# Kernel tuning notes

Measured on AMD Instinct MI355X. Metric: run time of the kernel, lower is better.

Reference implementation:

```python
import jax, jax.numpy as jnp
import numpy as np

X_DIM = 64
Y_DIM = 64
U_DIM = 64
BATCH = 32
SEQ_LEN = 2048
DT = 1.0 / 1024.0
EPS = 1e-4


def setup_inputs() -> dict:
    key = jax.random.key(0)
    k_y, k_a, k_c = jax.random.split(key, 3)
    y = jax.random.normal(k_y, (BATCH, SEQ_LEN, Y_DIM), dtype=jnp.float32)
    # parameters, matching the module's initialization (small noise added to A/C for generality)
    A = jnp.diag(-0.01 * (jnp.arange(X_DIM, dtype=jnp.float32) + 1.0)) \
        + 0.001 * jax.random.normal(k_a, (X_DIM, X_DIM), dtype=jnp.float32)
    B = jnp.eye(X_DIM, U_DIM, dtype=jnp.float32) * 0.1
    C = 0.1 * jax.random.normal(k_c, (Y_DIM, X_DIM), dtype=jnp.float32)
    L_Q = jnp.eye(X_DIM, dtype=jnp.float32) * 0.316
    L_R = jnp.eye(U_DIM, dtype=jnp.float32) * 0.316
    L_V = jnp.eye(Y_DIM, dtype=jnp.float32)
    L_Q_proc = jnp.eye(X_DIM, dtype=jnp.float32) * 0.1
    x0_mean = jnp.zeros((X_DIM,), dtype=jnp.float32)
    P0 = jnp.eye(X_DIM, dtype=jnp.float32) * 0.1
    return {"y": y, "A": A, "B": B, "C": C, "L_Q": L_Q, "L_R": L_R,
            "L_V": L_V, "L_Q_proc": L_Q_proc, "x0_mean": x0_mean, "P0": P0}


def _riccati_step(S, H, n):
    # Euler step of the augmented Hamiltonian flow; P = V @ U^{-1}
    S_new = S + DT * (H @ S)
    U, V = S_new[:n], S_new[n:]
    X = V @ jnp.linalg.inv(U)
    return X, S_new


def _forward(y, A, B, C, L_Q, L_R, L_V, L_Q_proc, x0_mean, P0):
    n = A.shape[0]
    u_dim = B.shape[1]
    y_dim = C.shape[0]
    batch, seq_len, _ = y.shape

    Q = L_Q @ L_Q.T
    R = L_R @ L_R.T
    V = L_V @ L_V.T
    Q_proc = L_Q_proc @ L_Q_proc.T

    # normalize observations (torch.std is unbiased -> ddof=1)
    y_mean = y.mean(axis=(0, 1), keepdims=True)
    y_std = y.std(axis=(0, 1), keepdims=True, ddof=1)
    yn = (y - y_mean) / (y_std + EPS)

    # --- LQR Riccati recursion: P_seq, K_seq (sequential scan over time) ---
    R_inv_reg = jnp.linalg.inv(R + EPS * jnp.eye(u_dim, dtype=R.dtype))
    H_care = jnp.block([[A, -B @ jnp.linalg.inv(R) @ B.T],
                        [-Q, -A.T]])  # augmented Hamiltonian (2n, 2n)

    def lqr_step(S, _):
        X, S_new = _riccati_step(S, H_care, n)
        P = 0.5 * (X + X.T)
        K = R_inv_reg @ (B.T @ P)  # (u_dim, n)
        return S_new, (P, K)

    S0 = jnp.concatenate([jnp.eye(n, dtype=Q.dtype), Q], axis=0)  # P0 = Q
    _, (P_seq, K_seq) = jax.lax.scan(lqr_step, S0, None, length=seq_len)

    # --- Kalman filter (sequential scan, data-dependent per-step linear algebra) ---
    V_reg = V + EPS * jnp.eye(y_dim, dtype=V.dtype)
    V_chol = jnp.linalg.cholesky(V_reg)
    log_det_V = 2.0 * jnp.sum(jnp.log(jnp.diagonal(V_chol)))
    Z = jnp.zeros((n, n), dtype=A.dtype)
    LOG_2PI = jnp.log(2.0 * jnp.pi).astype(A.dtype)

    def kf_step(carry, inp):
        x_t, S, ll = carry
        K_t, y_t = inp  # (u_dim, n), (batch, y_dim)
        A_eff = A - B @ K_t
        x_pred = x_t + DT * (x_t @ A_eff.T)  # (batch, n)
        H_t = jnp.block([[A_eff, Q_proc], [Z, -A_eff.T]])
        P_new, S = _riccati_step(S, H_t, n)
        P_pred = 0.5 * (P_new + P_new.T)
        residual = y_t - x_pred @ C.T  # (batch, y_dim)
        CtP = C @ P_pred  # (y_dim, n)
        Sm = CtP @ C.T + V
        S_inv = jnp.linalg.inv(Sm + EPS * jnp.eye(y_dim, dtype=Sm.dtype))
        Kg = CtP.T @ S_inv  # (n, y_dim)
        x_new = x_pred + residual @ Kg.T
        quad = jnp.sum(residual * (residual @ S_inv.T))  # sum_b r^T S_inv r
        ll = ll - 0.5 * (quad + log_det_V + y_dim * LOG_2PI)
        return (x_new, S, ll), x_new

    S0_kf = jnp.concatenate([jnp.eye(n, dtype=P0.dtype), P0], axis=0)
    x0 = jnp.broadcast_to(x0_mean, (batch, n))
    y_t_major = jnp.swapaxes(yn, 0, 1)  # (T, B, y_dim)
    (_, _, ll), x_filt_t = jax.lax.scan(kf_step, (x0, S0_kf, jnp.float32(0.0)),
                                        (K_seq, y_t_major))
    x_filt = jnp.swapaxes(x_filt_t, 0, 1)  # (B, T, n)
    log_likelihood = ll / seq_len

    # controls, prediction, quadratic costs (fully vectorized)
    u_seq = -jnp.einsum('tux,btx->btu', K_seq, x_filt)
    y_pred = x_filt @ C.T
    x_cost = jnp.einsum('btx,xz,btz->b', x_filt, Q, x_filt)
    u_cost = jnp.einsum('btu,uv,btv->b', u_seq, R, u_seq)
    control_cost = jnp.mean(x_cost + u_cost)
    return log_likelihood, control_cost, x_filt, u_seq, y_pred, yn


def reference(y, A, B, C, L_Q, L_R, L_V, L_Q_proc, x0_mean, P0):
    return _forward(y, A, B, C, L_Q, L_R, L_V, L_Q_proc, x0_mean, P0)
```

## Files before the change

kernel.cpp:

```cpp
#include <hip/hip_runtime.h>
#include <math.h>

#define XD 64
#define SEQL 2048
#define NB 32
#define DT_C  (1.0f/1024.0f)
#define EPS_C 1e-4f
#define LD 68
#define LOG2PI 1.8378770664093453f
#define CHUNK 8
#define NCH 256

#define OFF_PARTIAL 0u
#define OFF_MEAN    32768u
#define OFF_STD     32832u
#define OFF_Q       32896u
#define OFF_R       36992u
#define OFF_VM      41088u
#define OFF_QP      45184u
#define OFF_RIREG   49280u
#define OFF_LOGDET  53376u
#define OFF_CHAIN   53440u
#define OFF_POW     250048u
#define OFF_BOUNDS  1298624u
#define OFF_K       1568960u
#define OFF_AEFF    9957568u
#define OFF_UV      18346176u
#define OFF_G       35123392u
#define OFF_B       43512000u
#define OFF_OPS2    OFF_UV
#define OFF_OPS3G   47706304u
#define OFF_OPS3B   49803456u
#define OFF_SB2     50852032u
#define OFF_XB      52949184u
#define OFF_QUAD    53473472u
#define OFF_COST    53475520u
#define OFF_BRI     53541056u

#define OOFF_XF 2
#define OOFF_U  4194306
#define OOFF_YP 8388610
#define OOFF_YN 12582914

template<int KD>
__device__ __forceinline__ void mmNN(int t, float* __restrict__ out, int ldo,
    const float* __restrict__ A, int lda, const float* __restrict__ B, int ldb,
    const float* __restrict__ addC = nullptr, int ldc = 0, float alpha = 1.0f)
{
  const int r0 = (t >> 4) << 2, c0 = (t & 15) << 2;
  float acc[4][4] = {};
  for (int k = 0; k < KD; k += 4) {
    float a_[4][4];
    #pragma unroll
    for (int i = 0; i < 4; ++i) {
      const float4 x = *(const float4*)&A[(r0+i)*lda + k];
      a_[i][0]=x.x; a_[i][1]=x.y; a_[i][2]=x.z; a_[i][3]=x.w;
    }
    #pragma unroll
    for (int kk = 0; kk < 4; ++kk) {
      const float4 bv = *(const float4*)&B[(k+kk)*ldb + c0];
      #pragma unroll
      for (int i = 0; i < 4; ++i) {
        const float a = a_[i][kk];
        acc[i][0] += a*bv.x; acc[i][1] += a*bv.y; acc[i][2] += a*bv.z; acc[i][3] += a*bv.w;
      }
    }
  }
  #pragma unroll
  for (int i = 0; i < 4; ++i)
    #pragma unroll
    for (int j = 0; j < 4; ++j) {
      float v = alpha*acc[i][j];
      if (addC) v += addC[(r0+i)*ldc + (c0+j)];
      out[(r0+i)*ldo + (c0+j)] = v;
    }
}

template<int KD>
__device__ __forceinline__ void mmTA(int t, float* __restrict__ out, int ldo,
    const float* __restrict__ A, int lda, const float* __restrict__ B, int ldb,
    const float* __restrict__ addC = nullptr, int ldc = 0, float alpha = 1.0f)
{
  const int r0 = (t >> 4) << 2, c0 = (t & 15) << 2;
  float acc[4][4] = {};
  for (int k = 0; k < KD; k += 4) {
    #pragma unroll
    for (int kk = 0; kk < 4; ++kk) {
      const float4 av4 = *(const float4*)&A[(k+kk)*lda + r0];
      const float4 bv4 = *(const float4*)&B[(k+kk)*ldb + c0];
      const float av[4] = {av4.x, av4.y, av4.z, av4.w};
      const float bv[4] = {bv4.x, bv4.y, bv4.z, bv4.w};
      #pragma unroll
      for (int i = 0; i < 4; ++i)
        #pragma unroll
        for (int j = 0; j < 4; ++j)
          acc[i][j] += av[i]*bv[j];
    }
  }
  #pragma unroll
  for (int i = 0; i < 4; ++i)
    #pragma unroll
    for (int j = 0; j < 4; ++j) {
      float v = alpha*acc[i][j];
      if (addC) v += addC[(r0+i)*ldc + (c0+j)];
      out[(r0+i)*ldo + (c0+j)] = v;
    }
}

template<int KD>
__device__ __forceinline__ void mmTB(int t, float* __restrict__ out, int ldo,
    const float* __restrict__ A, int lda, const float* __restrict__ B, int ldb,
    const float* __restrict__ addC = nullptr, int ldc = 0, float alpha = 1.0f)
{
  const int r0 = (t >> 4) << 2, c0 = (t & 15) << 2;
  float acc[4][4] = {};
  for (int k = 0; k < KD; k += 4) {
    float a_[4][4], b_[4][4];
    #pragma unroll
    for (int i = 0; i < 4; ++i) {
      const float4 x = *(const float4*)&A[(r0+i)*lda + k];
      a_[i][0]=x.x; a_[i][1]=x.y; a_[i][2]=x.z; a_[i][3]=x.w;
    }
    #pragma unroll
    for (int j = 0; j < 4; ++j) {
      const float4 x = *(const float4*)&B[(c0+j)*ldb + k];
      b_[j][0]=x.x; b_[j][1]=x.y; b_[j][2]=x.z; b_[j][3]=x.w;
    }
    #pragma unroll
    for (int i = 0; i < 4; ++i)
      #pragma unroll
      for (int j = 0; j < 4; ++j)
        acc[i][j] += a_[i][0]*b_[j][0] + a_[i][1]*b_[j][1] + a_[i][2]*b_[j][2] + a_[i][3]*b_[j][3];
  }
  #pragma unroll
  for (int i = 0; i < 4; ++i)
    #pragma unroll
    for (int j = 0; j < 4; ++j) {
      float v = alpha*acc[i][j];
      if (addC) v += addC[(r0+i)*ldc + (c0+j)];
      out[(r0+i)*ldo + (c0+j)] = v;
    }
}

__device__ __forceinline__ void symTile(int t, float* __restrict__ outb, const float* __restrict__ X)
{
  const int r0 = (t >> 4) << 2, c0 = (t & 15) << 2;
  float xa[4][4], xb[4][4];
  #pragma unroll
  for (int i = 0; i < 4; ++i) {
    const float4 u = *(const float4*)&X[(r0+i)*LD + c0];
    xa[i][0]=u.x; xa[i][1]=u.y; xa[i][2]=u.z; xa[i][3]=u.w;
    const float4 v = *(const float4*)&X[(c0+i)*LD + r0];
    xb[i][0]=v.x; xb[i][1]=v.y; xb[i][2]=v.z; xb[i][3]=v.w;
  }
  #pragma unroll
  for (int i = 0; i < 4; ++i) {
    float4 o;
    o.x = 0.5f*(xa[i][0] + xb[0][i]);
    o.y = 0.5f*(xa[i][1] + xb[1][i]);
    o.z = 0.5f*(xa[i][2] + xb[2][i]);
    o.w = 0.5f*(xa[i][3] + xb[3][i]);
    *(float4*)&outb[(r0+i)*LD + c0] = o;
  }
}

template<int KD>
__device__ __forceinline__ void mm32NN(int t, float* __restrict__ out, int ldo,
    const float* __restrict__ A, int lda, const float* __restrict__ B, int ldb,
    const float* __restrict__ addC = nullptr, int ldc = 0, float alpha = 1.0f)
{
  const int r0 = (t >> 4) << 1, c0 = (t & 15) << 2;
  float acc[2][4] = {};
  for (int k = 0; k < KD; k += 4) {
    float a_[2][4];
    #pragma unroll
    for (int i = 0; i < 2; ++i) {
      const float4 x = *(const float4*)&A[(r0+i)*lda + k];
      a_[i][0]=x.x; a_[i][1]=x.y; a_[i][2]=x.z; a_[i][3]=x.w;
    }
    #pragma unroll
    for (int kk = 0; kk < 4; ++kk) {
      const float4 bv = *(const float4*)&B[(k+kk)*ldb + c0];
      #pragma unroll
      for (int i = 0; i < 2; ++i) {
        const float a = a_[i][kk];
        acc[i][0] += a*bv.x; acc[i][1] += a*bv.y; acc[i][2] += a*bv.z; acc[i][3] += a*bv.w;
      }
    }
  }
  #pragma unroll
  for (int i = 0; i < 2; ++i)
    #pragma unroll
    for (int j = 0; j < 4; ++j) {
      float v = alpha*acc[i][j];
      if (addC) v += addC[(r0+i)*ldc + (c0+j)];
      out[(r0+i)*ldo + (c0+j)] = v;
    }
}

template<int KD>
__device__ __forceinline__ void mm32TB(int t, float* __restrict__ out, int ldo,
    const float* __restrict__ A, size_t lda, const float* __restrict__ B, int ldb,
    const float* __restrict__ addC = nullptr, size_t ldc = 0, float alpha = 1.0f)
{
  const int r0 = (t >> 4) << 1, c0 = (t & 15) << 2;
  float acc[2][4] = {};
  for (int k = 0; k < KD; k += 4) {
    float a_[2][4], b_[4][4];
    #pragma unroll
    for (int i = 0; i < 2; ++i) {
      const float4 x = *(const float4*)&A[(size_t)(r0+i)*lda + k];
      a_[i][0]=x.x; a_[i][1]=x.y; a_[i][2]=x.z; a_[i][3]=x.w;
    }
    #pragma unroll
    for (int j = 0; j < 4; ++j) {
      const float4 x = *(const float4*)&B[(c0+j)*ldb + k];
      b_[j][0]=x.x; b_[j][1]=x.y; b_[j][2]=x.z; b_[j][3]=x.w;
    }
    #pragma unroll
    for (int i = 0; i < 2; ++i)
      #pragma unroll
      for (int j = 0; j < 4; ++j)
        acc[i][j] += a_[i][0]*b_[j][0] + a_[i][1]*b_[j][1] + a_[i][2]*b_[j][2] + a_[i][3]*b_[j][3];
  }
  #pragma unroll
  for (int i = 0; i < 2; ++i)
    #pragma unroll
    for (int j = 0; j < 4; ++j) {
      float v = alpha*acc[i][j];
      if (addC) v += addC[(size_t)(r0+i)*ldc + (c0+j)];
      out[(r0+i)*ldo + (c0+j)] = v;
    }
}

__device__ __forceinline__ void gj64(int t, float* __restrict__ Am, float* __restrict__ R)
{
  const int r = t >> 2;
  const int c0 = (t & 3) << 4;
  for (int k = 0; k < 64; ++k) {
    __syncthreads();
    const float pv = Am[k*LD + k];
    const float f = Am[r*LD + k] / pv;
    if (r != k) {
      #pragma unroll
      for (int c = 0; c < 16; c += 4) {
        float4 ak = *(const float4*)&Am[k*LD + c0 + c];
        float4 ar = *(float4*)&Am[r*LD + c0 + c];
        ar.x -= f*ak.x; ar.y -= f*ak.y; ar.z -= f*ak.z; ar.w -= f*ak.w;
        *(float4*)&Am[r*LD + c0 + c] = ar;
        float4 rk = *(const float4*)&R[k*LD + c0 + c];
        float4 rr = *(float4*)&R[r*LD + c0 + c];
        rr.x -= f*rk.x; rr.y -= f*rk.y; rr.z -= f*rk.z; rr.w -= f*rk.w;
        *(float4*)&R[r*LD + c0 + c] = rr;
      }
    }
  }
  __syncthreads();
  const float dinv = 1.0f / Am[r*LD + r];
  #pragma unroll
  for (int c = 0; c < 16; c += 4) {
    float4 rr = *(float4*)&R[r*LD + c0 + c];
    rr.x *= dinv; rr.y *= dinv; rr.z *= dinv; rr.w *= dinv;
    *(float4*)&R[r*LD + c0 + c] = rr;
  }
  __syncthreads();
}

__device__ __forceinline__ void gjb8(int t, float* __restrict__ Am, float* __restrict__ R)
{
  const int r  = t >> 2;
  const int c0 = (t & 3) << 4;
  const int j2 = t >> 5;
  const int cc = (t & 31) << 2;
  const int lane = t & 63;
  const int li = lane >> 3, lj = lane & 7;
  for (int kb = 0; kb < 8; ++kb) {
    const int K = kb << 3;
    __syncthreads();
    const bool inK = ((unsigned)(r - K)) < 8u;
    float4 f0 = make_float4(0.f,0.f,0.f,0.f), f1 = f0;
    if (!inK) {
      f0 = *(const float4*)&Am[r*LD + K];
      f1 = *(const float4*)&Am[r*LD + K + 4];
    }
    float a = Am[(K+li)*LD + K + lj];
    float w = (li == lj) ? 1.0f : 0.0f;
    #pragma unroll
    for (int p = 0; p < 8; ++p) {
      const float pv  = __shfl(a, p*8 + p, 64);
      const float pvr = __builtin_amdgcn_rcpf(pv);
      const float aip = __shfl(a, li*8 + p, 64);
      const float apj = __shfl(a, p*8 + lj, 64);
      const float wpj = __shfl(w, p*8 + lj, 64);
      const float fi  = aip * pvr;
      if (li == p) { a *= pvr; w *= pvr; }
      else         { a -= fi * apj; w -= fi * wpj; }
    }
    float wrow[8];
    #pragma unroll
    for (int m = 0; m < 8; ++m) wrow[m] = __shfl(w, j2*8 + m, 64);
    const int c4 = cc & 63;
    float* srcB = (cc < 64) ? Am : R;
    float4 acc = make_float4(0.f, 0.f, 0.f, 0.f);
    #pragma unroll
    for (int m = 0; m < 8; ++m) {
      const float4 rv = *(const float4*)&srcB[(K+m)*LD + c4];
      acc.x += wrow[m]*rv.x; acc.y += wrow[m]*rv.y; acc.z += wrow[m]*rv.z; acc.w += wrow[m]*rv.w;
    }
    __syncthreads();
    *(float4*)&srcB[(K+j2)*LD + c4] = acc;
    __syncthreads();
    if (!inK) {
      const float fj[8] = {f0.x, f0.y, f0.z, f0.w, f1.x, f1.y, f1.z, f1.w};
      #pragma unroll
      for (int c = 0; c < 16; c += 4) {
        const int cab = c0 + c;
        if (cab >= K + 8) {
          float4 v = *(float4*)&Am[r*LD + cab];
          #pragma unroll
          for (int j = 0; j < 8; ++j) {
            const float4 p4 = *(const float4*)&Am[(K+j)*LD + cab];
            v.x -= fj[j]*p4.x; v.y -= fj[j]*p4.y; v.z -= fj[j]*p4.z; v.w -= fj[j]*p4.w;
          }
          *(float4*)&Am[r*LD + cab] = v;
        }
      }
      #pragma unroll
      for (int c = 0; c < 16; c += 4) {
        const int cab = c0 + c;
        float4 v = *(float4*)&R[r*LD + cab];
        #pragma unroll
        for (int j = 0; j < 8; ++j) {
          const float4 p4 = *(const float4*)&R[(K+j)*LD + cab];
          v.x -= fj[j]*p4.x; v.y -= fj[j]*p4.y; v.z -= fj[j]*p4.z; v.w -= fj[j]*p4.w;
        }
        *(float4*)&R[r*LD + cab] = v;
      }
    }
  }
  __syncthreads();
}


__global__ __launch_bounds__(256) void k_stats(const float* __restrict__ y, float* __restrict__ ws)
{
  __shared__ float sbuf[4][128];
  const int t = threadIdx.x, blk = blockIdx.x;
  const int d = t & 63, g = t >> 6;
  float s = 0.f, s2 = 0.f;
  for (int r = g; r < 256; r += 4) {
    const float v = y[(size_t)(blk*256 + r)*64 + d];
    s += v; s2 += v*v;
  }
  sbuf[g][d] = s; sbuf[g][64+d] = s2;
  __syncthreads();
  if (t < 128) ws[OFF_PARTIAL + (size_t)blk*128 + t] = sbuf[0][t]+sbuf[1][t]+sbuf[2][t]+sbuf[3][t];
}

__global__ __launch_bounds__(256) void k_setup(
    const float* __restrict__ A, const float* __restrict__ Bi,
    const float* __restrict__ LQ, const float* __restrict__ LR,
    const float* __restrict__ LV, const float* __restrict__ LQp,
    float* __restrict__ ws)
{
  __shared__ float b1[64*LD], b2[64*LD], b3[64*LD], b4[64*LD], bQ[64*LD];
  __shared__ float sred[128];
  const int t = threadIdx.x;

  if (t < 128) {
    float acc = 0.f;
    for (int p = 0; p < 256; ++p) acc += ws[OFF_PARTIAL + (size_t)p*128 + t];
    sred[t] = acc;
  }
  __syncthreads();
  if (t < 64) {
    const float mean = sred[t] * (1.0f/65536.0f);
    const float var = (sred[64+t] - 65536.0f*mean*mean) * (1.0f/65535.0f);
    ws[OFF_MEAN + t] = mean;
    ws[OFF_STD + t] = sqrtf(var);
  }

  mmTB<64>(t, bQ, LD, LQ, 64, LQ, 64);
  mmTB<64>(t, b3, LD, LR, 64, LR, 64);
  mmTB<64>(t, ws+OFF_VM, 64, LV, 64, LV, 64);
  mmTB<64>(t, ws+OFF_QP, 64, LQp, 64, LQp, 64);
  __syncthreads();
  for (int idx = t; idx < 4096; idx += 256) {
    const int r = idx>>6, c = idx&63;
    ws[OFF_Q + idx] = bQ[r*LD+c];
    ws[OFF_R + idx] = b3[r*LD+c];
    b1[r*LD+c] = b3[r*LD+c] + ((r==c)?EPS_C:0.f);
    b2[r*LD+c] = (r==c)?1.f:0.f;
  }
  gj64(t, b1, b2);
  mmNN<64>(t, b4, LD, Bi, 64, b2, LD);
  __syncthreads();
  for (int idx = t; idx < 4096; idx += 256) {
    ws[OFF_RIREG + idx] = b2[(idx>>6)*LD+(idx&63)];
    ws[OFF_BRI + idx]   = b4[(idx>>6)*LD+(idx&63)];
  }
  __syncthreads();
  for (int idx = t; idx < 4096; idx += 256) {
    const int r = idx>>6, c = idx&63;
    b1[r*LD+c] = b3[r*LD+c];
    b2[r*LD+c] = (r==c)?1.f:0.f;
  }
  gj64(t, b1, b2);
  mmTB<64>(t, b3, LD, b2, LD, Bi, 64);
  __syncthreads();
  mmNN<64>(t, b4, LD, Bi, 64, b3, LD);
  mmTB<64>(t, b1, LD, LV, 64, LV, 64);
  __syncthreads();
  if (t < 64) b1[t*LD+t] += EPS_C;
  {
    const int r = t >> 2, c0 = (t & 3) << 4;
    float lsum = 0.f;
    for (int k = 0; k < 64; ++k) {
      __syncthreads();
      const float pv = b1[k*LD+k];
      lsum += logf(pv);
      const float f = b1[r*LD+k] / pv;
      if (r != k) {
        #pragma unroll
        for (int c = 0; c < 16; c += 4) {
          float4 ak = *(const float4*)&b1[k*LD+c0+c];
          float4 ar = *(float4*)&b1[r*LD+c0+c];
          ar.x -= f*ak.x; ar.y -= f*ak.y; ar.z -= f*ak.z; ar.w -= f*ak.w;
          *(float4*)&b1[r*LD+c0+c] = ar;
        }
      }
    }
    if (t == 0) ws[OFF_LOGDET] = lsum;
  }
  __syncthreads();
  float* M0 = ws + OFF_CHAIN;
  for (int idx = t; idx < 16384; idx += 256) {
    const int i = idx >> 7, j = idx & 127;
    float v;
    if (i < 64) v = (j < 64) ? (((i==j)?1.f:0.f) + DT_C*A[i*64+j]) : (-DT_C*b4[i*LD + (j-64)]);
    else        v = (j < 64) ? (-DT_C*bQ[(i-64)*LD + j]) : (((i==j)?1.f:0.f) - DT_C*A[(j-64)*64 + (i-64)]);
    M0[idx] = v;
  }
  for (int idx = t; idx < 16384; idx += 256) {
    const int i = idx >> 7, j = idx & 127;
    ws[OFF_POW + idx] = (i==j)?1.f:0.f;
  }
  for (int idx = t; idx < 8192; idx += 256) {
    const int i = idx >> 6, j = idx & 63;
    ws[OFF_BOUNDS + idx] = (i < 64) ? ((i==j)?1.f:0.f) : bQ[(i-64)*LD + j];
  }
}

__global__ __launch_bounds__(256) void k_yn(const float* __restrict__ y, const float* __restrict__ ws, float* __restrict__ out)
{
  const size_t i0 = ((size_t)blockIdx.x*256 + threadIdx.x)*4;
  const int d = (int)(i0 & 63);
  const float4 v = *(const float4*)&y[i0];
  const float4 m = *(const float4*)&ws[OFF_MEAN + d];
  const float4 s = *(const float4*)&ws[OFF_STD + d];
  float* o = out + OOFF_YN + i0;
  o[0] = (v.x - m.x)/(s.x + EPS_C);
  o[1] = (v.y - m.y)/(s.y + EPS_C);
  o[2] = (v.z - m.z)/(s.z + EPS_C);
  o[3] = (v.w - m.w)/(s.w + EPS_C);
}

__global__ __launch_bounds__(256) void k_sq(const float* __restrict__ src, float* __restrict__ dst)
{
  const int t = threadIdx.x;
  const int r = blockIdx.x*8 + (t >> 5);
  const int c0 = (t & 31) << 2;
  float acc[4] = {0.f,0.f,0.f,0.f};
  for (int k = 0; k < 128; k += 4) {
    const float4 a4 = *(const float4*)&src[r*128 + k];
    const float av[4] = {a4.x, a4.y, a4.z, a4.w};
    #pragma unroll
    for (int kk = 0; kk < 4; ++kk) {
      const float4 bv = *(const float4*)&src[(k+kk)*128 + c0];
      acc[0] += av[kk]*bv.x; acc[1] += av[kk]*bv.y; acc[2] += av[kk]*bv.z; acc[3] += av[kk]*bv.w;
    }
  }
  float4 o; o.x=acc[0]; o.y=acc[1]; o.z=acc[2]; o.w=acc[3];
  *(float4*)&dst[r*128 + c0] = o;
}

__global__ __launch_bounds__(256) void k_pow(const float* __restrict__ chainj, float* __restrict__ powt, int level)
{
  const int i = blockIdx.x >> 2, sub = blockIdx.x & 3;
  const float* Bm = powt + (size_t)i*16384;
  float* D = powt + (size_t)(i + (1<<level))*16384;
  const int t = threadIdx.x;
  const int r0 = sub*32 + ((t >> 4) << 1);
  const int c0 = (t & 15) << 3;
  float acc[2][8] = {};
  for (int k = 0; k < 128; k += 4) {
    float a_[2][4];
    {
      const float4 x = *(const float4*)&chainj[r0*128 + k];
      a_[0][0]=x.x; a_[0][1]=x.y; a_[0][2]=x.z; a_[0][3]=x.w;
      const float4 y2 = *(const float4*)&chainj[(r0+1)*128 + k];
      a_[1][0]=y2.x; a_[1][1]=y2.y; a_[1][2]=y2.z; a_[1][3]=y2.w;
    }
    #pragma unroll
    for (int kk = 0; kk < 4; ++kk) {
      const float4 b0 = *(const float4*)&Bm[(k+kk)*128 + c0];
      const float4 b1v = *(const float4*)&Bm[(k+kk)*128 + c0 + 4];
      #pragma unroll
      for (int i2 = 0; i2 < 2; ++i2) {
        const float a = a_[i2][kk];
        acc[i2][0] += a*b0.x; acc[i2][1] += a*b0.y; acc[i2][2] += a*b0.z; acc[i2][3] += a*b0.w;
        acc[i2][4] += a*b1v.x; acc[i2][5] += a*b1v.y; acc[i2][6] += a*b1v.z; acc[i2][7] += a*b1v.w;
      }
    }
  }
  #pragma unroll
  for (int i2 = 0; i2 < 2; ++i2)
    #pragma unroll
    for (int j = 0; j < 8; ++j)
      D[(r0+i2)*128 + c0 + j] = acc[i2][j];
}

__global__ __launch_bounds__(256) void k_boundsk(const float* __restrict__ chainp, float* __restrict__ ws, int level)
{
  const int kb = blockIdx.x >> 1, sub = blockIdx.x & 1;
  const int dsti = kb + (1 << level);
  if (dsti > 32) return;
  const float* S = ws + OFF_BOUNDS + (size_t)kb*8192;
  float* D = ws + OFF_BOUNDS + (size_t)dsti*8192;
  const int t = threadIdx.x;
  const int r0 = sub*64 + ((t >> 4) << 2);
  const int c0 = (t & 15) << 2;
  float acc[4][4] = {};
  for (int k = 0; k < 128; k += 4) {
    float a_[4][4];
    #pragma unroll
    for (int i = 0; i < 4; ++i) {
      const float4 x = *(const float4*)&chainp[(r0+i)*128 + k];
      a_[i][0]=x.x; a_[i][1]=x.y; a_[i][2]=x.z; a_[i][3]=x.w;
    }
    #pragma unroll
    for (int kk = 0; kk < 4; ++kk) {
      const float4 bv = *(const float4*)&S[(k+kk)*64 + c0];
      #pragma unroll
      for (int i = 0; i < 4; ++i) {
        const float a = a_[i][kk];
        acc[i][0] += a*bv.x; acc[i][1] += a*bv.y; acc[i][2] += a*bv.z; acc[i][3] += a*bv.w;
      }
    }
  }
  #pragma unroll
  for (int i = 0; i < 4; ++i)
    #pragma unroll
    for (int j = 0; j < 4; ++j)
      D[(r0+i)*64 + c0 + j] = acc[i][j];
}

__global__ __launch_bounds__(256) void k_lqr(const float* __restrict__ Ain, const float* __restrict__ Bin, float* __restrict__ ws)
{
  __shared__ float b1[64*LD], b2[64*LD], b3[64*LD];
  const int t = threadIdx.x, tt = blockIdx.x;
  const int tp1 = tt + 1, kc = tp1 >> 6, rr = tp1 & 63;
  const float* Mr = ws + OFF_POW + (size_t)rr*16384;
  const float* SB = ws + OFF_BOUNDS + (size_t)kc*8192;
  mmNN<128>(t, b1, LD, Mr, 128, SB, 64);
  mmNN<128>(t, b3, LD, Mr + 8192, 128, SB, 64);
  for (int idx = t; idx < 4096; idx += 256) {
    const int r = idx>>6, c = idx&63;
    b2[r*LD+c] = (r==c)?1.f:0.f;
  }
  gjb8(t, b1, b2);
  mmNN<64>(t, b1, LD, b3, LD, b2, LD);
  __syncthreads();
  symTile(t, b3, b1);
  __syncthreads();
  mmTA<64>(t, b1, LD, Bin, 64, b3, LD);
  __syncthreads();
  mmNN<64>(t, b2, LD, ws+OFF_RIREG, 64, b1, LD);
  mmNN<64>(t, b3, LD, ws+OFF_BRI, 64, b1, LD);
  __syncthreads();
  float* Kout = ws + OFF_K + (size_t)tt*4096;
  float* Ae   = ws + OFF_AEFF + (size_t)tt*4096;
  for (int idx = t; idx < 4096; idx += 256) {
    const int p = (idx>>6)*LD + (idx&63);
    Kout[idx] = b2[p];
    Ae[idx]   = Ain[idx] - b3[p];
  }
}

__global__ __launch_bounds__(1024) void k_ops2(const float* __restrict__ ws_aeff, const float* __restrict__ ws_qp, float* __restrict__ dstE)
{
  __shared__ float E[64*LD], W[64*LD], F[64*LD], T1[64*LD], T2[64*LD], T3[64*LD], T4[64*LD];
  const int t = threadIdx.x, c = blockIdx.x, g = t >> 8, tl = t & 255;
  for (int idx = t; idx < 4096; idx += 1024) {
    const int r = idx>>6, cc = idx&63; const float id = (r==cc)?1.f:0.f;
    E[r*LD+cc] = id; W[r*LD+cc] = 0.f; F[r*LD+cc] = id;
  }
  __syncthreads();
  for (int s = 0; s < CHUNK; ++s) {
    const float* Ae = ws_aeff + ((size_t)c*CHUNK + s)*4096;
    if (g == 0)      mmNN<64>(tl, T1, LD, Ae, 64, E, LD);
    else if (g == 1) mmNN<64>(tl, T2, LD, Ae, 64, W, LD);
    else if (g == 2) mmNN<64>(tl, T3, LD, ws_qp, 64, F, LD);
    else             mmTA<64>(tl, T4, LD, Ae, 64, F, LD);
    __syncthreads();
    for (int idx = t; idx < 4096; idx += 1024) {
      const int p = (idx>>6)*LD + (idx&63);
      E[p] += DT_C*T1[p];
      W[p] += DT_C*(T2[p] + T3[p]);
      F[p] -= DT_C*T4[p];
    }
    __syncthreads();
  }
  float* dst = dstE + (size_t)c*12288;
  for (int idx = t; idx < 4096; idx += 1024) {
    const int p = (idx>>6)*LD + (idx&63);
    dst[idx] = E[p]; dst[4096+idx] = W[p]; dst[8192+idx] = F[p];
  }
}

__global__ __launch_bounds__(1024) void k_scan2(const float* __restrict__ src, float* __restrict__ dst, int s)
{
  __shared__ float t1[64*LD], t2[64*LD];
  const int i = blockIdx.x, t = threadIdx.x, g = t>>8, tl = t&255;
  const float* si = src + (size_t)i*12288;
  float* di = dst + (size_t)i*12288;
  if (i < s) {
    for (int idx = t; idx < 12288; idx += 1024) di[idx] = si[idx];
    return;
  }
  const float* sj = src + (size_t)(i-s)*12288;
  if (g == 0)      mmNN<64>(tl, di, 64, si, 64, sj, 64);
  else if (g == 1) mmNN<64>(tl, t1, LD, si, 64, sj+4096, 64);
  else if (g == 2) mmNN<64>(tl, t2, LD, si+4096, 64, sj+8192, 64);
  else             mmNN<64>(tl, di+8192, 64, si+8192, 64, sj+8192, 64);
  __syncthreads();
  for (int idx = t; idx < 4096; idx += 1024) {
    const int p = (idx>>6)*LD + (idx&63);
    di[4096+idx] = t1[p] + t2[p];
  }
}

__global__ __launch_bounds__(256) void k_sb2(const float* __restrict__ phi, const float* __restrict__ P0, float* __restrict__ ws)
{
  const int c = blockIdx.x, t = threadIdx.x;
  float* D = ws + OFF_SB2 + (size_t)c*8192;
  if (c == 0) {
    for (int idx = t; idx < 4096; idx += 256) {
      const int r = idx>>6, cc = idx&63;
      D[idx] = (r==cc)?1.f:0.f;
      D[4096+idx] = P0[idx];
    }
    return;
  }
  const float* ph = phi + (size_t)(c-1)*12288;
  mmNN<64>(t, D, 64, ph+4096, 64, P0, 64, ph, 64);
  mmNN<64>(t, D+4096, 64, ph+8192, 64, P0, 64);
}

__global__ __launch_bounds__(1024) void k_uvwalk(const float* __restrict__ ws_aeff, const float* __restrict__ ws_qp,
    const float* __restrict__ ws_sb2, float* __restrict__ ws_uv)
{
  __shared__ float U[64*LD], V[64*LD], T1[64*LD], T2[64*LD], T3[64*LD];
  const int c = blockIdx.x, t = threadIdx.x, g = t>>8, tl = t&255;
  const float* S = ws_sb2 + (size_t)c*8192;
  for (int idx = t; idx < 4096; idx += 1024) {
    const int p = (idx>>6)*LD + (idx&63);
    U[p] = S[idx]; V[p] = S[4096+idx];
  }
  __syncthreads();
  for (int s = 0; s < CHUNK; ++s) {
    const size_t tt = (size_t)c*CHUNK + s;
    const float* Ae = ws_aeff + tt*4096;
    if (g == 0)      mmNN<64>(tl, T1, LD, Ae, 64, U, LD);
    else if (g == 1) mmNN<64>(tl, T2, LD, ws_qp, 64, V, LD);
    else if (g == 2) mmTA<64>(tl, T3, LD, Ae, 64, V, LD);
    __syncthreads();
    float* O = ws_uv + tt*8192;
    for (int idx = t; idx < 4096; idx += 1024) {
      const int p = (idx>>6)*LD + (idx&63);
      const float un = U[p] + DT_C*(T1[p] + T2[p]);
      const float vn = V[p] - DT_C*T3[p];
      U[p] = un; V[p] = vn;
      O[idx] = un; O[4096+idx] = vn;
    }
    __syncthreads();
  }
}

__global__ __launch_bounds__(256) void k_kfper(const float* __restrict__ Cin, const float* __restrict__ outyn, float* __restrict__ ws)
{
  __shared__ float b1[64*LD], b2[64*LD], b3[64*LD];
  const int t = threadIdx.x, tt = blockIdx.x;
  float* base = ws + OFF_UV + (size_t)tt*8192;
  for (int idx = t; idx < 4096; idx += 256) {
    const int r = idx>>6, c = idx&63;
    b1[r*LD+c] = base[idx];
    b3[r*LD+c] = base[4096+idx];
    b2[r*LD+c] = (r==c)?1.f:0.f;
  }
  gjb8(t, b1, b2);
  mmNN<64>(t, b1, LD, b3, LD, b2, LD);
  __syncthreads();
  symTile(t, b3, b1);
  __syncthreads();
  mmNN<64>(t, b1, LD, Cin, 64, b3, LD);
  __syncthreads();
  mmTB<64>(t, b2, LD, b1, LD, Cin, 64, ws+OFF_VM, 64);
  __syncthreads();
  if (t < 64) b2[t*LD+t] += EPS_C;
  for (int idx = t; idx < 4096; idx += 256) {
    const int r = idx>>6, c = idx&63;
    b3[r*LD+c] = (r==c)?1.f:0.f;
  }
  gjb8(t, b2, b3);
  for (int idx = t; idx < 4096; idx += 256) base[4096+idx] = b3[(idx>>6)*LD+(idx&63)];
  mmTA<64>(t, b2, LD, b1, LD, b3, LD);
  __syncthreads();
  for (int idx = t; idx < 4096; idx += 256) base[idx] = b2[(idx>>6)*LD+(idx&63)];
  mmNN<64>(t, b3, LD, b2, LD, Cin, 64);
  __syncthreads();
  const float* Ae = ws + OFF_AEFF + (size_t)tt*4096;
  float* Gg = ws + OFF_G + (size_t)tt*4096;
  {
    const int r0 = (t>>4)<<2, cg0 = (t&15)<<2;
    float acc[4][4] = {};
    for (int k = 0; k < 64; k += 4) {
      float a_[4][4];
      #pragma unroll
      for (int kk = 0; kk < 4; ++kk) {
        const float4 x = *(const float4*)&Ae[(k+kk)*64 + r0];
        a_[kk][0]=x.x; a_[kk][1]=x.y; a_[kk][2]=x.z; a_[kk][3]=x.w;
      }
      float yv[4][4];
      #pragma unroll
      for (int j = 0; j < 4; ++j) {
        const float4 z4 = *(const float4*)&b3[(cg0+j)*LD + k];
        yv[j][0] = -z4.x; yv[j][1] = -z4.y; yv[j][2] = -z4.z; yv[j][3] = -z4.w;
        const int dk = (cg0+j) - k;
        if (dk >= 0 && dk < 4) yv[j][dk] += 1.0f;
      }
      #pragma unroll
      for (int kk = 0; kk < 4; ++kk)
        #pragma unroll
        for (int i = 0; i < 4; ++i) {
          const float a = a_[kk][i];
          #pragma unroll
          for (int j = 0; j < 4; ++j) acc[i][j] += a * yv[j][kk];
        }
    }
    #pragma unroll
    for (int i = 0; i < 4; ++i)
      #pragma unroll
      for (int j = 0; j < 4; ++j) {
        const int rw = r0+i, cw = cg0+j;
        const float Yij = ((rw==cw)?1.f:0.f) - b3[cw*LD + rw];
        b1[rw*LD+cw] = Yij + DT_C*acc[i][j];
      }
  }
  __syncthreads();
  for (int idx = t; idx < 4096; idx += 256) Gg[idx] = b1[(idx>>6)*LD+(idx&63)];
  mm32TB<64>(t, b3, LD, outyn + (size_t)tt*64, (size_t)131072, b2, LD);
  __syncthreads();
  float* Bout = ws + OFF_B + (size_t)tt*2048;
  for (int idx = t; idx < 2048; idx += 256) Bout[idx] = b3[(idx>>6)*LD+(idx&63)];
}

__global__ __launch_bounds__(1024) void k_ops3(const float* __restrict__ ws_g, const float* __restrict__ ws_b,
    float* __restrict__ dG, float* __restrict__ dB)
{
  __shared__ float Gc[64*LD], TG[64*LD], bc[NB*LD], Tb[NB*LD];
  const int t = threadIdx.x, c = blockIdx.x, g = t >> 8, tl = t & 255;
  for (int idx = t; idx < 4096; idx += 1024) {
    const int r = idx>>6, cc = idx&63;
    Gc[r*LD+cc] = (r==cc)?1.f:0.f;
  }
  for (int idx = t; idx < 2048; idx += 1024) bc[(idx>>6)*LD+(idx&63)] = 0.f;
  __syncthreads();
  for (int s = 0; s < CHUNK; ++s) {
    const size_t tt = (size_t)c*CHUNK + s;
    const float* Gt = ws_g + tt*4096;
    if (g == 0)      mmNN<64>(tl, TG, LD, Gc, LD, Gt, 64);
    else if (g == 1) mm32NN<64>(tl, Tb, LD, bc, LD, Gt, 64);
    __syncthreads();
    for (int idx = t; idx < 4096; idx += 1024) {
      const int p = (idx>>6)*LD + (idx&63);
      Gc[p] = TG[p];
    }
    const float* bt = ws_b + tt*2048;
    for (int idx = t; idx < 2048; idx += 1024) {
      const int p = (idx>>6)*LD + (idx&63);
      bc[p] = Tb[p] + bt[idx];
    }
    __syncthreads();
  }
  for (int idx = t; idx < 4096; idx += 1024) dG[(size_t)c*4096 + idx] = Gc[(idx>>6)*LD+(idx&63)];
  for (int idx = t; idx < 2048; idx += 1024) dB[(size_t)c*2048 + idx] = bc[(idx>>6)*LD+(idx&63)];
}

__global__ __launch_bounds__(512) void k_scan3(const float* __restrict__ sG, const float* __restrict__ sB,
    float* __restrict__ dG, float* __restrict__ dB, int s)
{
  const int i = blockIdx.x, t = threadIdx.x, g = t>>8, tl = t&255;
  if (i < s) {
    for (int idx = t; idx < 4096; idx += 512) dG[(size_t)i*4096+idx] = sG[(size_t)i*4096+idx];
    for (int idx = t; idx < 2048; idx += 512) dB[(size_t)i*2048+idx] = sB[(size_t)i*2048+idx];
    return;
  }
  const float* Ge = sG + (size_t)(i-s)*4096;
  const float* Gl = sG + (size_t)i*4096;
  if (g == 0) mmNN<64>(tl, dG + (size_t)i*4096, 64, Ge, 64, Gl, 64);
  else        mm32NN<64>(tl, dB + (size_t)i*2048, 64, sB + (size_t)(i-s)*2048, 64, Gl, 64,
                         sB + (size_t)i*2048, 64);
}

__global__ __launch_bounds__(256) void k_xb(const float* __restrict__ phiG, const float* __restrict__ phiB,
    const float* __restrict__ x0, float* __restrict__ ws)
{
  __shared__ float v[64];
  const int c = blockIdx.x, t = threadIdx.x;
  float* D = ws + OFF_XB + (size_t)c*2048;
  if (c == 0) {
    for (int idx = t; idx < 2048; idx += 256) D[idx] = x0[idx&63];
    return;
  }
  const float* G = phiG + (size_t)(c-1)*4096;
  const float* b = phiB + (size_t)(c-1)*2048;
  if (t < 64) {
    float acc = 0.f;
    for (int k = 0; k < 64; ++k) acc += x0[k]*G[k*64 + t];
    v[t] = acc;
  }
  __syncthreads();
  for (int idx = t; idx < 2048; idx += 256) D[idx] = v[idx&63] + b[idx];
}

__global__ __launch_bounds__(256) void k_xwalk(const float* __restrict__ ws_g, const float* __restrict__ ws_b,
    const float* __restrict__ ws_xb, float* __restrict__ outx)
{
  __shared__ float x[NB*LD], xn[NB*LD];
  const int c = blockIdx.x, t = threadIdx.x;
  const float* X0 = ws_xb + (size_t)c*2048;
  for (int idx = t; idx < 2048; idx += 256) x[(idx>>6)*LD+(idx&63)] = X0[idx];
  __syncthreads();
  for (int s = 0; s < CHUNK; ++s) {
    const size_t tt = (size_t)c*CHUNK + s;
    mm32NN<64>(t, xn, LD, x, LD, ws_g + tt*4096, 64, ws_b + tt*2048, 64);
    __syncthreads();
    for (int idx = t; idx < 2048; idx += 256) {
      const int i = idx>>6, d = idx&63;
      const float val = xn[i*LD+d];
      x[i*LD+d] = val;
      outx[(size_t)i*131072 + tt*64 + d] = val;
    }
    __syncthreads();
  }
}

__global__ __launch_bounds__(256) void k_final(const float* __restrict__ Cin, const float* __restrict__ x0,
    const float* __restrict__ outx, const float* __restrict__ outyn,
    float* __restrict__ outu, float* __restrict__ outyp, float* __restrict__ ws)
{
  __shared__ float xc[NB*LD], z[NB*LD], t1[NB*LD], t2[NB*LD];
  __shared__ float red4[4];
  const int tt = blockIdx.x, t = threadIdx.x;
  for (int idx = t; idx < 2048; idx += 256) {
    const int i = idx>>6, d = idx&63;
    xc[i*LD+d] = outx[(size_t)i*131072 + (size_t)tt*64 + d];
    z[i*LD+d]  = (tt == 0) ? x0[d] : outx[(size_t)i*131072 + (size_t)(tt-1)*64 + d];
  }
  __syncthreads();
  mm32TB<64>(t, t1, LD, xc, LD, ws + OFF_K + (size_t)tt*4096, 64, nullptr, 0, -1.0f);
  mm32TB<64>(t, t2, LD, xc, LD, Cin, 64);
  __syncthreads();
  for (int idx = t; idx < 2048; idx += 256) {
    const int i = idx>>6, d = idx&63;
    outu[(size_t)i*131072 + (size_t)tt*64 + d]  = t1[i*LD+d];
    outyp[(size_t)i*131072 + (size_t)tt*64 + d] = t2[i*LD+d];
  }
  __syncthreads();
  mm32NN<64>(t, t2, LD, xc, LD, ws + OFF_Q, 64);
  __syncthreads();
  const int i_ = t >> 3, lane8 = t & 7;
  float cpart = 0.f;
  for (int d = lane8; d < 64; d += 8) cpart += t2[i_*LD+d]*xc[i_*LD+d];
  __syncthreads();
  mm32NN<64>(t, t2, LD, t1, LD, ws + OFF_R, 64);
  __syncthreads();
  for (int d = lane8; d < 64; d += 8) cpart += t2[i_*LD+d]*t1[i_*LD+d];
  cpart += __shfl_down(cpart, 4, 8);
  cpart += __shfl_down(cpart, 2, 8);
  cpart += __shfl_down(cpart, 1, 8);
  if (lane8 == 0) ws[OFF_COST + (size_t)tt*32 + i_] = cpart;
  __syncthreads();
  mm32TB<64>(t, t2, LD, z, LD, ws + OFF_AEFF + (size_t)tt*4096, 64, z, LD, DT_C);
  __syncthreads();
  mm32TB<64>(t, t1, LD, t2, LD, Cin, 64, outyn + (size_t)tt*64, (size_t)131072, -1.0f);
  __syncthreads();
  mm32TB<64>(t, z, LD, t1, LD, ws + OFF_UV + (size_t)tt*8192 + 4096, 64);
  __syncthreads();
  float q = 0.f;
  for (int idx = t; idx < 2048; idx += 256) {
    const int p = (idx>>6)*LD + (idx&63);
    q += t1[p]*z[p];
  }
  q += __shfl_down(q, 32); q += __shfl_down(q, 16); q += __shfl_down(q, 8);
  q += __shfl_down(q, 4);  q += __shfl_down(q, 2);  q += __shfl_down(q, 1);
  if ((t & 63) == 0) red4[t>>6] = q;
  __syncthreads();
  if (t == 0) ws[OFF_QUAD + tt] = red4[0]+red4[1]+red4[2]+red4[3];
}

__global__ __launch_bounds__(256) void k_scalars(const float* __restrict__ ws, float* __restrict__ out)
{
  __shared__ float red[256];
  const int t = threadIdx.x;
  float q = 0.f;
  for (int i = t; i < 2048; i += 256) q += ws[OFF_QUAD + i];
  red[t] = q;
  __syncthreads();
  for (int s = 128; s > 0; s >>= 1) { if (t < s) red[t] += red[t+s]; __syncthreads(); }
  const float quadsum = red[0];
  __syncthreads();
  {
    const int b = t & 31, chunk = t >> 5;
    float a = 0.f;
    for (int j = 0; j < 256; ++j) a += ws[OFF_COST + (size_t)(chunk*256 + j)*32 + b];
    red[t] = a;
  }
  __syncthreads();
  if (t < 32) {
    float a = 0.f;
    for (int ch = 0; ch < 8; ++ch) a += red[ch*32 + t];
    red[t] = a;
  }
  __syncthreads();
  if (t == 0) {
    float cc = 0.f;
    for (int b = 0; b < 32; ++b) cc += red[b];
    out[1] = cc / 32.0f;
    const float ld = ws[OFF_LOGDET];
    out[0] = -0.5f*(quadsum + 2048.0f*(ld + 64.0f*LOG2PI)) / 2048.0f;
  }
}

extern "C" void kernel_launch(void* const* d_in, const int* in_sizes, int n_in,
                              void* d_out, int out_size, void* d_ws, size_t ws_size,
                              hipStream_t stream)
{
  (void)in_sizes; (void)n_in; (void)out_size; (void)ws_size;
  const float* y   = (const float*)d_in[0];
  const float* A   = (const float*)d_in[1];
  const float* Bi  = (const float*)d_in[2];
  const float* C   = (const float*)d_in[3];
  const float* LQ  = (const float*)d_in[4];
  const float* LR  = (const float*)d_in[5];
  const float* LV  = (const float*)d_in[6];
  const float* LQp = (const float*)d_in[7];
  const float* x0  = (const float*)d_in[8];
  const float* P0  = (const float*)d_in[9];
  float* out = (float*)d_out;
  float* ws  = (float*)d_ws;

  k_stats<<<256, 256, 0, stream>>>(y, ws);
  k_setup<<<1, 256, 0, stream>>>(A, Bi, LQ, LR, LV, LQp, ws);
  k_yn<<<4096, 256, 0, stream>>>(y, ws, out);

  for (int j = 1; j <= 11; ++j)
    k_sq<<<16, 256, 0, stream>>>(ws + OFF_CHAIN + (size_t)(j-1)*16384, ws + OFF_CHAIN + (size_t)j*16384);
  for (int j = 0; j <= 5; ++j)
    k_pow<<<4 << j, 256, 0, stream>>>(ws + OFF_CHAIN + (size_t)j*16384, ws + OFF_POW, j);
  for (int j = 0; j <= 5; ++j)
    k_boundsk<<<2 << j, 256, 0, stream>>>(ws + OFF_CHAIN + (size_t)(6+j)*16384, ws, j);

  k_lqr<<<2048, 256, 0, stream>>>(A, Bi, ws);

  k_ops2<<<NCH, 1024, 0, stream>>>(ws + OFF_AEFF, ws + OFF_QP, ws + OFF_OPS2);
  {
    float* pa = ws + OFF_OPS2;
    float* pb = pa + (size_t)NCH*12288;
    float* src = pa; float* dst = pb;
    for (int s = 1; s < NCH; s <<= 1) {
      k_scan2<<<NCH, 1024, 0, stream>>>(src, dst, s);
      float* tmp = src; src = dst; dst = tmp;
    }
    k_sb2<<<NCH, 256, 0, stream>>>(src, P0, ws);
  }
  k_uvwalk<<<NCH, 1024, 0, stream>>>(ws + OFF_AEFF, ws + OFF_QP, ws + OFF_SB2, ws + OFF_UV);
  k_kfper<<<2048, 256, 0, stream>>>(C, out + OOFF_YN, ws);

  k_ops3<<<NCH, 1024, 0, stream>>>(ws + OFF_G, ws + OFF_B, ws + OFF_OPS3G, ws + OFF_OPS3B);
  {
    float* ga = ws + OFF_OPS3G; float* gb = ga + (size_t)NCH*4096;
    float* ba = ws + OFF_OPS3B; float* bb = ba + (size_t)NCH*2048;
    float *gs = ga, *gd = gb, *bs = ba, *bd = bb;
    for (int s = 1; s < NCH; s <<= 1) {
      k_scan3<<<NCH, 512, 0, stream>>>(gs, bs, gd, bd, s);
      float* t1p = gs; gs = gd; gd = t1p;
      float* t2p = bs; bs = bd; bd = t2p;
    }
    k_xb<<<NCH, 256, 0, stream>>>(gs, bs, x0, ws);
  }
  k_xwalk<<<NCH, 256, 0, stream>>>(ws + OFF_G, ws + OFF_B, ws + OFF_XB, out + OOFF_XF);

  k_final<<<2048, 256, 0, stream>>>(C, x0, out + OOFF_XF, out + OOFF_YN, out + OOFF_U, out + OOFF_YP, ws);
  k_scalars<<<1, 256, 0, stream>>>(ws, out);
}
```

Before: 2.356 ms.

## Fuse repeated-squaring chain into one LDS kernel and merge pow/bounds launches

Replaces 11 separate k_sq launches with a single 1024-thread block that keeps the 128x128 matrix in shared memory (128 KB across two buffers) and squares it repeatedly, writing each power to global. It also merges the k_pow and k_boundsk launches for each level into one k_powbounds launch, since the two are independent. This cuts roughly 17 kernel launches and their serialisation gaps. In exchange the squaring runs on a single CU, and it needs 128 KB of LDS, which must fit the device limit.

Result: slower. 2.459 ms (+4.4%).

```diff
diff --git a/kernel.cpp b/kernel.cpp
--- a/kernel.cpp
+++ b/kernel.cpp
@@ -465,94 +465,110 @@
   o[3] = (v.w - m.w)/(s.w + EPS_C);
 }
 
-__global__ __launch_bounds__(256) void k_sq(const float* __restrict__ src, float* __restrict__ dst)
-{
+__global__ __launch_bounds__(1024) void k_sqchain(float* __restrict__ chain)
+{
+  __shared__ float bufA[128*128], bufB[128*128];
   const int t = threadIdx.x;
-  const int r = blockIdx.x*8 + (t >> 5);
-  const int c0 = (t & 31) << 2;
-  float acc[4] = {0.f,0.f,0.f,0.f};
-  for (int k = 0; k < 128; k += 4) {
-    const float4 a4 = *(const float4*)&src[r*128 + k];
-    const float av[4] = {a4.x, a4.y, a4.z, a4.w};
-    #pragma unroll
-    for (int kk = 0; kk < 4; ++kk) {
-      const float4 bv = *(const float4*)&src[(k+kk)*128 + c0];
-      acc[0] += av[kk]*bv.x; acc[1] += av[kk]*bv.y; acc[2] += av[kk]*bv.z; acc[3] += av[kk]*bv.w;
-    }
-  }
-  float4 o; o.x=acc[0]; o.y=acc[1]; o.z=acc[2]; o.w=acc[3];
-  *(float4*)&dst[r*128 + c0] = o;
-}
-
-__global__ __launch_bounds__(256) void k_pow(const float* __restrict__ chainj, float* __restrict__ powt, int level)
-{
-  const int i = blockIdx.x >> 2, sub = blockIdx.x & 3;
-  const float* Bm = powt + (size_t)i*16384;
-  float* D = powt + (size_t)(i + (1<<level))*16384;
+  for (int idx = t; idx < 16384; idx += 1024) bufA[idx] = chain[idx];
+  __syncthreads();
+  float* Abuf = bufA; float* Bbuf = bufB;
+  for (int j = 1; j <= 11; ++j) {
+    float* dst = chain + (size_t)j*16384;
+    const int c0 = (t & 31) << 2;
+    #pragma unroll
+    for (int g = 0; g < 4; ++g) {
+      const int r = (t >> 5) + (g << 5);
+      float a0=0.f, a1=0.f, a2=0.f, a3=0.f;
+      for (int k = 0; k < 128; k += 4) {
+        const float4 a4 = *(const float4*)&Abuf[r*128 + k];
+        const float av[4] = {a4.x, a4.y, a4.z, a4.w};
+        #pragma unroll
+        for (int kk = 0; kk < 4; ++kk) {
+          const float4 b4 = *(const float4*)&Abuf[(k+kk)*128 + c0];
+          a0 += av[kk]*b4.x; a1 += av[kk]*b4.y; a2 += av[kk]*b4.z; a3 += av[kk]*b4.w;
+        }
+      }
+      float4 o; o.x=a0; o.y=a1; o.z=a2; o.w=a3;
+      *(float4*)&Bbuf[r*128 + c0] = o;
+      *(float4*)&dst[r*128 + c0] = o;
+    }
+    __syncthreads();
+    float* tmp = Abuf; Abuf = Bbuf; Bbuf = tmp;
+  }
+}
+
+__global__ __launch_bounds__(256) void k_powbounds(const float* __restrict__ chain, float* __restrict__ ws, int level)
+{
+  const int nbp = 4 << level;
   const int t = threadIdx.x;
-  const int r0 = sub*32 + ((t >> 4) << 1);
-  const int c0 = (t & 15) << 3;
-  float acc[2][8] = {};
-  for (int k = 0; k < 128; k += 4) {
-    float a_[2][4];
-    {
-      const float4 x = *(const float4*)&chainj[r0*128 + k];
-      a_[0][0]=x.x; a_[0][1]=x.y; a_[0][2]=x.z; a_[0][3]=x.w;
-      const float4 y2 = *(const float4*)&chainj[(r0+1)*128 + k];
-      a_[1][0]=y2.x; a_[1][1]=y2.y; a_[1][2]=y2.z; a_[1][3]=y2.w;
-    }
-    #pragma unroll
-    for (int kk = 0; kk < 4; ++kk) {
-      const float4 b0 = *(const float4*)&Bm[(k+kk)*128 + c0];
-      const float4 b1v = *(const float4*)&Bm[(k+kk)*128 + c0 + 4];
-      #pragma unroll
-      for (int i2 = 0; i2 < 2; ++i2) {
-        const float a = a_[i2][kk];
-        acc[i2][0] += a*b0.x; acc[i2][1] += a*b0.y; acc[i2][2] += a*b0.z; acc[i2][3] += a*b0.w;
-        acc[i2][4] += a*b1v.x; acc[i2][5] += a*b1v.y; acc[i2][6] += a*b1v.z; acc[i2][7] += a*b1v.w;
-      }
-    }
-  }
-  #pragma unroll
-  for (int i2 = 0; i2 < 2; ++i2)
-    #pragma unroll
-    for (int j = 0; j < 8; ++j)
-      D[(r0+i2)*128 + c0 + j] = acc[i2][j];
-}
-
-__global__ __launch_bounds__(256) void k_boundsk(const float* __restrict__ chainp, float* __restrict__ ws, int level)
-{
-  const int kb = blockIdx.x >> 1, sub = blockIdx.x & 1;
-  const int dsti = kb + (1 << level);
-  if (dsti > 32) return;
-  const float* S = ws + OFF_BOUNDS + (size_t)kb*8192;
-  float* D = ws + OFF_BOUNDS + (size_t)dsti*8192;
-  const int t = threadIdx.x;
-  const int r0 = sub*64 + ((t >> 4) << 2);
-  const int c0 = (t & 15) << 2;
-  float acc[4][4] = {};
-  for (int k = 0; k < 128; k += 4) {
-    float a_[4][4];
-    #pragma unroll
-    for (int i = 0; i < 4; ++i) {
-      const float4 x = *(const float4*)&chainp[(r0+i)*128 + k];
-      a_[i][0]=x.x; a_[i][1]=x.y; a_[i][2]=x.z; a_[i][3]=x.w;
-    }
-    #pragma unroll
-    for (int kk = 0; kk < 4; ++kk) {
-      const float4 bv = *(const float4*)&S[(k+kk)*64 + c0];
+  if ((int)blockIdx.x < nbp) {
+    const float* chainj = chain + (size_t)level*16384;
+    float* powt = ws + OFF_POW;
+    const int i = blockIdx.x >> 2, sub = blockIdx.x & 3;
+    const float* Bm = powt + (size_t)i*16384;
+    float* D = powt + (size_t)(i + (1<<level))*16384;
+    const int r0 = sub*32 + ((t >> 4) << 1);
+    const int c0 = (t & 15) << 3;
+    float acc[2][8] = {};
+    for (int k = 0; k < 128; k += 4) {
+      float a_[2][4];
+      {
+        const float4 x = *(const float4*)&chainj[r0*128 + k];
+        a_[0][0]=x.x; a_[0][1]=x.y; a_[0][2]=x.z; a_[0][3]=x.w;
+        const float4 y2 = *(const float4*)&chainj[(r0+1)*128 + k];
+        a_[1][0]=y2.x; a_[1][1]=y2.y; a_[1][2]=y2.z; a_[1][3]=y2.w;
+      }
+      #pragma unroll
+      for (int kk = 0; kk < 4; ++kk) {
+        const float4 b0 = *(const float4*)&Bm[(k+kk)*128 + c0];
+        const float4 b1v = *(const float4*)&Bm[(k+kk)*128 + c0 + 4];
+        #pragma unroll
+        for (int i2 = 0; i2 < 2; ++i2) {
+          const float a = a_[i2][kk];
+          acc[i2][0] += a*b0.x; acc[i2][1] += a*b0.y; acc[i2][2] += a*b0.z; acc[i2][3] += a*b0.w;
+          acc[i2][4] += a*b1v.x; acc[i2][5] += a*b1v.y; acc[i2][6] += a*b1v.z; acc[i2][7] += a*b1v.w;
+        }
+      }
+    }
+    #pragma unroll
+    for (int i2 = 0; i2 < 2; ++i2)
+      #pragma unroll
+      for (int j = 0; j < 8; ++j)
+        D[(r0+i2)*128 + c0 + j] = acc[i2][j];
+  } else {
+    const int bb = blockIdx.x - nbp;
+    const int kb = bb >> 1, sub = bb & 1;
+    const int dsti = kb + (1 << level);
+    if (dsti > 32) return;
+    const float* chainp = chain + (size_t)(6+level)*16384;
+    const float* S = ws + OFF_BOUNDS + (size_t)kb*8192;
+    float* D = ws + OFF_BOUNDS + (size_t)dsti*8192;
+    const int r0 = sub*64 + ((t >> 4) << 2);
+    const int c0 = (t & 15) << 2;
+    float acc[4][4] = {};
+    for (int k = 0; k < 128; k += 4) {
+      float a_[4][4];
       #pragma unroll
       for (int i = 0; i < 4; ++i) {
-        const float a = a_[i][kk];
-        acc[i][0] += a*bv.x; acc[i][1] += a*bv.y; acc[i][2] += a*bv.z; acc[i][3] += a*bv.w;
-      }
-    }
-  }
-  #pragma unroll
-  for (int i = 0; i < 4; ++i)
-    #pragma unroll
-    for (int j = 0; j < 4; ++j)
-      D[(r0+i)*64 + c0 + j] = acc[i][j];
+        const float4 x = *(const float4*)&chainp[(r0+i)*128 + k];
+        a_[i][0]=x.x; a_[i][1]=x.y; a_[i][2]=x.z; a_[i][3]=x.w;
+      }
+      #pragma unroll
+      for (int kk = 0; kk < 4; ++kk) {
+        const float4 bv = *(const float4*)&S[(k+kk)*64 + c0];
+        #pragma unroll
+        for (int i = 0; i < 4; ++i) {
+          const float a = a_[i][kk];
+          acc[i][0] += a*bv.x; acc[i][1] += a*bv.y; acc[i][2] += a*bv.z; acc[i][3] += a*bv.w;
+        }
+      }
+    }
+    #pragma unroll
+    for (int i = 0; i < 4; ++i)
+      #pragma unroll
+      for (int j = 0; j < 4; ++j)
+        D[(r0+i)*64 + c0 + j] = acc[i][j];
+  }
 }
 
 __global__ __launch_bounds__(256) void k_lqr(const float* __restrict__ Ain, const float* __restrict__ Bin, float* __restrict__ ws)
@@ -965,12 +981,9 @@
   k_setup<<<1, 256, 0, stream>>>(A, Bi, LQ, LR, LV, LQp, ws);
   k_yn<<<4096, 256, 0, stream>>>(y, ws, out);
 
-  for (int j = 1; j <= 11; ++j)
-    k_sq<<<16, 256, 0, stream>>>(ws + OFF_CHAIN + (size_t)(j-1)*16384, ws + OFF_CHAIN + (size_t)j*16384);
+  k_sqchain<<<1, 1024, 0, stream>>>(ws + OFF_CHAIN);
   for (int j = 0; j <= 5; ++j)
-    k_pow<<<4 << j, 256, 0, stream>>>(ws + OFF_CHAIN + (size_t)j*16384, ws + OFF_POW, j);
-  for (int j = 0; j <= 5; ++j)
-    k_boundsk<<<2 << j, 256, 0, stream>>>(ws + OFF_CHAIN + (size_t)(6+j)*16384, ws, j);
+    k_powbounds<<<6 << j, 256, 0, stream>>>(ws + OFF_CHAIN, ws, j);
 
   k_lqr<<<2048, 256, 0, stream>>>(A, Bi, ws);
 
```
